# Optimization experiments

Measured on AMD Instinct MI355X. Metric: run time of the kernel, lower is better.

Reference implementation:

```python
import jax, jax.numpy as jnp
import numpy as np
import math

B, N, OBS, ACT = 128, 64, 128, 16
D = OBS + ACT          # obs_act_input_dim = 144
DK = 128               # obs_act_output_dim (d_k)
ENC = 128              # encoder_output_dim
FIN = 1                # final_output_dim


def setup_inputs() -> dict:
    key = jax.random.key(0)
    ks = jax.random.split(key, 8)
    s = 0.05
    return {
        "observations": jax.random.normal(ks[0], (B, N, OBS), jnp.float32),
        "policies": jax.random.uniform(ks[1], (B, N, ACT), jnp.float32),
        "actions": jax.random.uniform(ks[2], (B, N, ACT), jnp.float32),
        # torch nn.Linear weights are [out, in]
        "Wk": jax.random.normal(ks[3], (DK, D), jnp.float32) * s,
        "Wq": jax.random.normal(ks[4], (DK, D), jnp.float32) * s,
        "Wv": jax.random.normal(ks[5], (DK, D), jnp.float32) * s,
        "Wenc": jax.random.normal(ks[6], (ENC, OBS), jnp.float32) * s,
        "Wfin": jax.random.normal(ks[7], (FIN, ENC + DK), jnp.float32) * s,
    }


def reference(observations, policies, actions, Wk, Wq, Wv, Wenc, Wfin):
    b, n = observations.shape[0], observations.shape[1]
    d_k = Wk.shape[0]
    oa = jnp.concatenate([observations, actions], axis=-1)      # [B,N,D]
    op = jnp.concatenate([observations, policies], axis=-1)     # [B,N,D]
    k = oa @ Wk.T                                               # [B,N,dk]
    q = oa @ Wq.T                                               # [B,N,dk]
    # torch: bmm(q, k^T).transpose(1,2) -> scores[b,i,j] = q[b,j] . k[b,i]
    scores = jnp.einsum('bjd,bid->bij', q, k)
    w = jax.nn.sigmoid(scores / math.sqrt(d_k))                 # [B,N,N]
    Va = oa @ Wv.T                                              # [B,N,dk] value of obs||action
    Vp = op @ Wv.T                                              # [B,N,dk] value of obs||policy
    # original 5D masked combine reduces to: agg[b,i,m] = (sum_j w[b,i,j]*Va[b,j]
    #   + w[b,i,m]*(Vp[b,m]-Va[b,m])) / N  (policy substituted only where j==m)
    S = jnp.einsum('bij,bjd->bid', w, Va)                       # [B,N,dk]
    agg = (S[:, :, None, :] + w[..., None] * (Vp - Va)[:, None, :, :]) / n  # [B,N,N,dk]
    enc = observations @ Wenc.T                                 # [B,N,ENC]
    enc_rep = jnp.broadcast_to(enc[:, :, None, :], (b, n, n, enc.shape[-1]))
    node = jnp.concatenate([enc_rep, agg], axis=-1)             # [B,N,N,ENC+dk]
    value = node @ Wfin.T                                       # [B,N,N,1]
    weights5 = jnp.broadcast_to(w[:, :, None, :, None], (b, n, n, n, 1))
    return value, weights5
```

## Files before the change

### kernel.cpp

```cpp
#include <hip/hip_runtime.h>
#include <stdint.h>


#define BB 128
#define NN 64
#define OBSD 128
#define ACTD 16
#define DD 144
#define DKD 128
#define RS 168

typedef float f32x4 __attribute__((ext_vector_type(4)));
typedef short bf16x8 __attribute__((ext_vector_type(8)));

#define WS_QT  1048576
#define WS_VAS 2097152
#define WS_VE  (WS_VAS + 8192)
#define WS_DV  (WS_VAS + 16384)

__device__ __forceinline__ unsigned int pack_bf2(float x, float y) {
  unsigned a = __float_as_uint(x), b = __float_as_uint(y);
  a = (a + 0x7fffu + ((a >> 16) & 1u)) >> 16;
  b = (b + 0x7fffu + ((b >> 16) & 1u)) >> 16;
  return a | (b << 16);
}
__device__ __forceinline__ float bf2f(unsigned short s) {
  return __uint_as_float(((unsigned)s) << 16);
}

__global__ __launch_bounds__(512, 2) void critic_kq(
    const float* __restrict__ obs, const float* __restrict__ pol, const float* __restrict__ act,
    const float* __restrict__ Wk, const float* __restrict__ Wq, const float* __restrict__ Wv,
    const float* __restrict__ Wenc, const float* __restrict__ Wfin,
    float* __restrict__ ws)
{
  __shared__ __align__(16) unsigned short s_A[NN * RS];
  __shared__ __align__(16) unsigned short s_B[DKD * RS];
  __shared__ float s_dpa[NN][ACTD];
  __shared__ float s_u[DD];
  __shared__ float s_g[OBSD];

  const int tid = threadIdx.x;
  const int b = blockIdx.x >> 1;
  const int half = blockIdx.x & 1;

  {
    const float4* obs4 = (const float4*)(obs + (size_t)b * NN * OBSD);
    for (int idx = tid; idx < 2048; idx += 512) {
      float4 v = obs4[idx];
      int row = idx >> 5, c4 = (idx & 31) * 4;
      *(uint2*)&s_A[row * RS + c4] = make_uint2(pack_bf2(v.x, v.y), pack_bf2(v.z, v.w));
    }
    const float4* act4 = (const float4*)(act + (size_t)b * NN * ACTD);
    const float4* pol4 = (const float4*)(pol + (size_t)b * NN * ACTD);
    for (int idx = tid; idx < 256; idx += 512) {
      float4 a = act4[idx];
      int row = idx >> 2, c4 = OBSD + (idx & 3) * 4;
      *(uint2*)&s_A[row * RS + c4] = make_uint2(pack_bf2(a.x, a.y), pack_bf2(a.z, a.w));
      if (half == 0) {
        float4 p = pol4[idx];
        int t0 = (idx & 3) * 4;
        s_dpa[row][t0 + 0] = p.x - a.x; s_dpa[row][t0 + 1] = p.y - a.y;
        s_dpa[row][t0 + 2] = p.z - a.z; s_dpa[row][t0 + 3] = p.w - a.w;
      }
    }
    for (int idx = tid; idx < 256; idx += 512) {
      int row = idx >> 2, c4 = DD + (idx & 3) * 4;
      *(uint2*)&s_A[row * RS + c4] = make_uint2(0u, 0u);
    }
  }
  {
    const float4* W4 = (const float4*)(half ? Wq : Wk);
    for (int idx = tid; idx < 4096; idx += 512) {
      int row = idx >> 5, g = idx & 31;
      float4 v = W4[row * 36 + g];
      *(uint2*)&s_B[row * RS + g * 4] = make_uint2(pack_bf2(v.x, v.y), pack_bf2(v.z, v.w));
    }
    for (int idx = tid; idx < 512; idx += 512) {
      int row = idx >> 2, g = idx & 3;
      float4 v = W4[row * 36 + 32 + g];
      *(uint2*)&s_B[row * RS + OBSD + g * 4] = make_uint2(pack_bf2(v.x, v.y), pack_bf2(v.z, v.w));
    }
    for (int idx = tid; idx < 512; idx += 512) {
      int row = idx >> 2, c4 = DD + (idx & 3) * 4;
      *(uint2*)&s_B[row * RS + c4] = make_uint2(0u, 0u);
    }
  }
  if (half == 0) {
    if (tid < DD) {
      float a0=0.f,a1=0.f,a2=0.f,a3=0.f,a4=0.f,a5=0.f,a6=0.f,a7=0.f;
      for (int c = 0; c < DKD; c += 8) {
        a0 += Wv[(size_t)(c+0)*DD + tid] * Wfin[OBSD + c + 0];
        a1 += Wv[(size_t)(c+1)*DD + tid] * Wfin[OBSD + c + 1];
        a2 += Wv[(size_t)(c+2)*DD + tid] * Wfin[OBSD + c + 2];
        a3 += Wv[(size_t)(c+3)*DD + tid] * Wfin[OBSD + c + 3];
        a4 += Wv[(size_t)(c+4)*DD + tid] * Wfin[OBSD + c + 4];
        a5 += Wv[(size_t)(c+5)*DD + tid] * Wfin[OBSD + c + 5];
        a6 += Wv[(size_t)(c+6)*DD + tid] * Wfin[OBSD + c + 6];
        a7 += Wv[(size_t)(c+7)*DD + tid] * Wfin[OBSD + c + 7];
      }
      s_u[tid] = ((a0+a1)+(a2+a3)) + ((a4+a5)+(a6+a7));
    } else if (tid < DD + OBSD) {
      const int d = tid - DD;
      float a0=0.f,a1=0.f,a2=0.f,a3=0.f,a4=0.f,a5=0.f,a6=0.f,a7=0.f;
      for (int c = 0; c < 128; c += 8) {
        a0 += Wenc[(size_t)(c+0)*OBSD + d] * Wfin[c + 0];
        a1 += Wenc[(size_t)(c+1)*OBSD + d] * Wfin[c + 1];
        a2 += Wenc[(size_t)(c+2)*OBSD + d] * Wfin[c + 2];
        a3 += Wenc[(size_t)(c+3)*OBSD + d] * Wfin[c + 3];
        a4 += Wenc[(size_t)(c+4)*OBSD + d] * Wfin[c + 4];
        a5 += Wenc[(size_t)(c+5)*OBSD + d] * Wfin[c + 5];
        a6 += Wenc[(size_t)(c+6)*OBSD + d] * Wfin[c + 6];
        a7 += Wenc[(size_t)(c+7)*OBSD + d] * Wfin[c + 7];
      }
      s_g[d] = ((a0+a1)+(a2+a3)) + ((a4+a5)+(a6+a7));
    }
  }
  __syncthreads();

  {
    const int wv = tid >> 6, lane = tid & 63;
    const int i0 = (wv & 3) * 16;
    const int n0 = (wv >> 2) * 4;
    const int m = lane & 15, q = lane >> 4;
    f32x4 acc[4];
    #pragma unroll
    for (int t = 0; t < 4; ++t) acc[t] = (f32x4){0.f, 0.f, 0.f, 0.f};
    #pragma unroll
    for (int ks = 0; ks < 5; ++ks) {
      const int koff = ks * 32 + q * 8;
      bf16x8 a = *(const bf16x8*)&s_A[(i0 + m) * RS + koff];
      #pragma unroll
      for (int t = 0; t < 4; ++t) {
        bf16x8 bb = *(const bf16x8*)&s_B[((n0 + t) * 16 + m) * RS + koff];
        acc[t] = __builtin_amdgcn_mfma_f32_16x16x32_bf16(a, bb, acc[t], 0, 0, 0);
      }
    }
    if (half == 0) {
      float* kb = ws + (size_t)b * 8192;
      #pragma unroll
      for (int t = 0; t < 4; ++t)
        #pragma unroll
        for (int r = 0; r < 4; ++r)
          kb[(i0 + q * 4 + r) * 128 + (n0 + t) * 16 + m] = acc[t][r];
    } else {
      float* qb = ws + WS_QT + (size_t)b * 8192;
      #pragma unroll
      for (int t = 0; t < 4; ++t)
        *(f32x4*)&qb[((n0 + t) * 16 + m) * 64 + i0 + q * 4] = acc[t];
    }
  }

  if (half == 0) {
    if (tid < 64) {
      float a = 0.f;
      for (int d = 0; d < DD; ++d) a += bf2f(s_A[tid * RS + d]) * s_u[d];
      ws[WS_VAS + b * 64 + tid] = a;
    } else if (tid < 128) {
      const int i = tid - 64;
      float a = 0.f;
      for (int d = 0; d < OBSD; ++d) a += bf2f(s_A[i * RS + d]) * s_g[d];
      ws[WS_VE + b * 64 + i] = a;
    } else if (tid < 192) {
      const int i = tid - 128;
      float a = 0.f;
      #pragma unroll
      for (int t = 0; t < ACTD; ++t) a += s_dpa[i][t] * s_u[OBSD + t];
      ws[WS_DV + b * 64 + i] = a;
    }
  }
}

__global__ __launch_bounds__(256, 3) void critic_sw(
    const float* __restrict__ ws, float* __restrict__ out)
{
  __shared__ __align__(16) float s_qT[DKD][64];
  __shared__ __align__(16) float s_k[16][132];
  __shared__ __align__(16) float s_w[16][68];
  __shared__ float s_vas[64], s_dv[64], s_ve[16], s_sv[16];

  const int t = threadIdx.x;
  const int b = blockIdx.x >> 2;
  const int i0 = (blockIdx.x & 3) * 16;

  {
    const float4* qt4 = (const float4*)(ws + WS_QT + (size_t)b * 8192);
    for (int idx = t; idx < 2048; idx += 256) {
      int c = idx >> 4, i4 = (idx & 15) * 4;
      *(float4*)&s_qT[c][i4] = qt4[idx];
    }
    const float4* k4 = (const float4*)(ws + (size_t)b * 8192 + (size_t)i0 * 128);
    for (int idx = t; idx < 512; idx += 256) {
      int r = idx >> 5, c4 = (idx & 31) * 4;
      *(float4*)&s_k[r][c4] = k4[idx];
    }
    if (t < 64)            s_vas[t] = ws[WS_VAS + b * 64 + t];
    else if (t < 128)      s_dv[t - 64] = ws[WS_DV + b * 64 + (t - 64)];
    else if (t < 144)      s_ve[t - 128] = ws[WS_VE + b * 64 + i0 + (t - 128)];
  }
  __syncthreads();

  {
    const int wv = t >> 6, j = t & 63;
    float sc0 = 0.f, sc1 = 0.f, sc2 = 0.f, sc3 = 0.f;
    #pragma unroll 4
    for (int d0 = 0; d0 < DKD; d0 += 4) {
      float q0 = s_qT[d0 + 0][j], q1 = s_qT[d0 + 1][j];
      float q2 = s_qT[d0 + 2][j], q3 = s_qT[d0 + 3][j];
      float4 k0 = *(const float4*)&s_k[wv * 4 + 0][d0];
      float4 k1 = *(const float4*)&s_k[wv * 4 + 1][d0];
      float4 k2 = *(const float4*)&s_k[wv * 4 + 2][d0];
      float4 k3 = *(const float4*)&s_k[wv * 4 + 3][d0];
      sc0 += k0.x * q0 + k0.y * q1 + k0.z * q2 + k0.w * q3;
      sc1 += k1.x * q0 + k1.y * q1 + k1.z * q2 + k1.w * q3;
      sc2 += k2.x * q0 + k2.y * q1 + k2.z * q2 + k2.w * q3;
      sc3 += k3.x * q0 + k3.y * q1 + k3.z * q2 + k3.w * q3;
    }
    const float kk = 0.08838834764831845f;
    s_w[wv * 4 + 0][j] = 1.0f / (1.0f + __expf(-sc0 * kk));
    s_w[wv * 4 + 1][j] = 1.0f / (1.0f + __expf(-sc1 * kk));
    s_w[wv * 4 + 2][j] = 1.0f / (1.0f + __expf(-sc2 * kk));
    s_w[wv * 4 + 3][j] = 1.0f / (1.0f + __expf(-sc3 * kk));
  }
  __syncthreads();

  if (t < 16) {
    float a = 0.f;
    for (int j = 0; j < 64; ++j) a += s_w[t][j] * s_vas[j];
    s_sv[t] = a;
  }
  __syncthreads();

  {
    const int r = t >> 4, m4 = (t & 15) * 4;
    float4 v;
    v.x = s_ve[r] + (s_sv[r] + s_w[r][m4 + 0] * s_dv[m4 + 0]) * (1.0f / 64.0f);
    v.y = s_ve[r] + (s_sv[r] + s_w[r][m4 + 1] * s_dv[m4 + 1]) * (1.0f / 64.0f);
    v.z = s_ve[r] + (s_sv[r] + s_w[r][m4 + 2] * s_dv[m4 + 2]) * (1.0f / 64.0f);
    v.w = s_ve[r] + (s_sv[r] + s_w[r][m4 + 3] * s_dv[m4 + 3]) * (1.0f / 64.0f);
    *(float4*)(out + ((size_t)(b * 64 + i0 + r) * 64 + m4)) = v;
  }

  float* w5 = out + (size_t)BB * NN * NN;
  #pragma unroll 4
  for (int r = 0; r < 16; ++r) {
    const float4 wv4 = *(const float4*)&s_w[r][(t & 15) * 4];
    float4* p4 = (float4*)(w5 + ((size_t)(b * 64 + i0 + r) << 12));
    p4[t]       = wv4;
    p4[t + 256] = wv4;
    p4[t + 512] = wv4;
    p4[t + 768] = wv4;
  }
}

extern "C" void kernel_launch(void* const* d_in, const int* in_sizes, int n_in,
                              void* d_out, int out_size, void* d_ws, size_t ws_size,
                              hipStream_t stream) {
  (void)in_sizes; (void)n_in; (void)out_size; (void)ws_size;
  const float* obs  = (const float*)d_in[0];
  const float* pol  = (const float*)d_in[1];
  const float* act  = (const float*)d_in[2];
  const float* Wk   = (const float*)d_in[3];
  const float* Wq   = (const float*)d_in[4];
  const float* Wv   = (const float*)d_in[5];
  const float* Wenc = (const float*)d_in[6];
  const float* Wfin = (const float*)d_in[7];
  float* out = (float*)d_out;
  float* ws  = (float*)d_ws;
  hipLaunchKernelGGL(critic_kq, dim3(BB * 2), dim3(512), 0, stream,
                     obs, pol, act, Wk, Wq, Wv, Wenc, Wfin, ws);
  hipLaunchKernelGGL(critic_sw, dim3(BB * 4), dim3(256), 0, stream, ws, out);
}
```

Baseline: 175.3 us.

## Split weight broadcast into a separate wide grid-stride kernel

The score kernel now writes the compact sigmoid weight matrix to workspace instead of directly writing the 64x-replicated 5D weights output. A new kernel with many more blocks reads the compact weights and performs the large broadcast store with a grid-stride loop. The aim is to spread the dominant output write across more threads and blocks to improve memory bandwidth use. The cost is an extra launch and a small intermediate round-trip through global memory.

```diff
diff --git a/kernel.cpp b/kernel.cpp
--- a/kernel.cpp
+++ b/kernel.cpp
@@ -17,6 +17,7 @@
 #define WS_VAS 2097152
 #define WS_VE  (WS_VAS + 8192)
 #define WS_DV  (WS_VAS + 16384)
+#define WS_W   (WS_VAS + 32768)
 
 __device__ __forceinline__ unsigned int pack_bf2(float x, float y) {
   unsigned a = __float_as_uint(x), b = __float_as_uint(y);
@@ -171,8 +172,8 @@
   }
 }
 
-__global__ __launch_bounds__(256, 3) void critic_sw(
-    const float* __restrict__ ws, float* __restrict__ out)
+__global__ __launch_bounds__(256, 3) void critic_w(
+    const float* __restrict__ ws_in, float* __restrict__ ws_w, float* __restrict__ out)
 {
   __shared__ __align__(16) float s_qT[DKD][64];
   __shared__ __align__(16) float s_k[16][132];
@@ -184,19 +185,19 @@
   const int i0 = (blockIdx.x & 3) * 16;
 
   {
-    const float4* qt4 = (const float4*)(ws + WS_QT + (size_t)b * 8192);
+    const float4* qt4 = (const float4*)(ws_in + WS_QT + (size_t)b * 8192);
     for (int idx = t; idx < 2048; idx += 256) {
       int c = idx >> 4, i4 = (idx & 15) * 4;
       *(float4*)&s_qT[c][i4] = qt4[idx];
     }
-    const float4* k4 = (const float4*)(ws + (size_t)b * 8192 + (size_t)i0 * 128);
+    const float4* k4 = (const float4*)(ws_in + (size_t)b * 8192 + (size_t)i0 * 128);
     for (int idx = t; idx < 512; idx += 256) {
       int r = idx >> 5, c4 = (idx & 31) * 4;
       *(float4*)&s_k[r][c4] = k4[idx];
     }
-    if (t < 64)            s_vas[t] = ws[WS_VAS + b * 64 + t];
-    else if (t < 128)      s_dv[t - 64] = ws[WS_DV + b * 64 + (t - 64)];
-    else if (t < 144)      s_ve[t - 128] = ws[WS_VE + b * 64 + i0 + (t - 128)];
+    if (t < 64)            s_vas[t] = ws_in[WS_VAS + b * 64 + t];
+    else if (t < 128)      s_dv[t - 64] = ws_in[WS_DV + b * 64 + (t - 64)];
+    else if (t < 144)      s_ve[t - 128] = ws_in[WS_VE + b * 64 + i0 + (t - 128)];
   }
   __syncthreads();
 
@@ -241,15 +242,21 @@
     *(float4*)(out + ((size_t)(b * 64 + i0 + r) * 64 + m4)) = v;
   }
 
-  float* w5 = out + (size_t)BB * NN * NN;
-  #pragma unroll 4
-  for (int r = 0; r < 16; ++r) {
-    const float4 wv4 = *(const float4*)&s_w[r][(t & 15) * 4];
-    float4* p4 = (float4*)(w5 + ((size_t)(b * 64 + i0 + r) << 12));
-    p4[t]       = wv4;
-    p4[t + 256] = wv4;
-    p4[t + 512] = wv4;
-    p4[t + 768] = wv4;
+  for (int idx = t; idx < 1024; idx += 256) {
+    int r = idx >> 6, j = idx & 63;
+    ws_w[(size_t)(b * 64 + i0 + r) * 64 + j] = s_w[r][j];
+  }
+}
+
+__global__ __launch_bounds__(256, 4) void critic_bc(
+    const float* __restrict__ ws_w, float* __restrict__ out)
+{
+  const float4* w4 = (const float4*)ws_w;
+  float4* o4 = (float4*)(out + (size_t)BB * NN * NN);
+  const unsigned total = 8388608u;
+  const unsigned stride = gridDim.x * blockDim.x;
+  for (unsigned f = blockIdx.x * blockDim.x + threadIdx.x; f < total; f += stride) {
+    o4[f] = w4[((f >> 10) << 4) + (f & 15)];
   }
 }
 
@@ -269,5 +276,8 @@
   float* ws  = (float*)d_ws;
   hipLaunchKernelGGL(critic_kq, dim3(BB * 2), dim3(512), 0, stream,
                      obs, pol, act, Wk, Wq, Wv, Wenc, Wfin, ws);
-  hipLaunchKernelGGL(critic_sw, dim3(BB * 4), dim3(256), 0, stream, ws, out);
-}
+  hipLaunchKernelGGL(critic_w, dim3(BB * 4), dim3(256), 0, stream,
+                     ws, ws + WS_W, out);
+  hipLaunchKernelGGL(critic_bc, dim3(4096), dim3(256), 0, stream,
+                     ws + WS_W, out);
+}
```

Measured after the change: 179.7 us. 2.5% more time.
